# Performance work log

Measured on AMD Instinct MI355X. Metric: run time of the kernel, lower is better.

The kernel has to match this reference:

```python
import jax, jax.numpy as jnp
import numpy as np

EMBED = 1024
HEADS = 16
HEAD_DIM = EMBED // HEADS


def setup_inputs() -> dict:
    key = jax.random.key(0)
    ks = jax.random.split(key, 6)
    N, S = 4, 1024
    query = jax.random.normal(ks[0], (N, S, EMBED), dtype=jnp.float32)
    keys = jax.random.normal(ks[1], (N, S, EMBED), dtype=jnp.float32)
    values = jax.random.normal(ks[2], (N, S, EMBED), dtype=jnp.float32)
    mask = jax.random.randint(ks[3], (N, 1, S, S), 0, 2, dtype=jnp.int32)
    W_out = jax.random.normal(ks[4], (EMBED, EMBED), dtype=jnp.float32) * (1.0 / np.sqrt(EMBED))
    b_out = jax.random.normal(ks[5], (EMBED,), dtype=jnp.float32) * 0.02
    return {"query": query, "keys": keys, "values": values, "mask": mask,
            "W_out": W_out, "b_out": b_out}


def reference(query, keys, values, mask, W_out, b_out):
    N, Q, _ = query.shape
    K = keys.shape[1]
    # NOTE: the torch module never applies its per-head q/k/v Linear layers;
    # only the reshape + attention + fc_out are in the forward path.
    q = query.reshape(N, Q, HEADS, HEAD_DIM)
    k = keys.reshape(N, K, HEADS, HEAD_DIM)
    v = values.reshape(N, K, HEADS, HEAD_DIM)
    # energy: [N, H, Q, K]
    energy = jnp.einsum("bqhd,bkhd->bhqk", q, k)
    energy = jnp.where(mask == 0, jnp.float32(-1e20), energy)
    attn = jax.nn.softmax(energy / jnp.sqrt(jnp.float32(HEAD_DIM)), axis=3)
    out = jnp.einsum("bhqk,bkhd->bqhd", attn, v).reshape(N, Q, HEADS * HEAD_DIM)
    return out @ W_out.T + b_out
```

## Files before the change

kernel.cpp:

```cpp
#include <hip/hip_runtime.h>
#include <math.h>

#define NB 4
#define SL 1024
#define EMB 1024
#define NH 16
#define HD 64
#define QB 128

typedef __attribute__((ext_vector_type(8))) short bf16x8;
typedef __attribute__((ext_vector_type(4))) float f32x4;
typedef __attribute__((ext_vector_type(4))) unsigned u32x4;

static __device__ __forceinline__ unsigned pk2(float a, float b) {
    unsigned x = __float_as_uint(a) + 0x8000u;
    unsigned y = __float_as_uint(b) + 0x8000u;
    return (x >> 16) | (y & 0xFFFF0000u);
}
static __device__ __forceinline__ float exp2_fast(float x) {
    float r; asm("v_exp_f32 %0, %1" : "=v"(r) : "v"(x)); return r;
}
static __device__ __forceinline__ unsigned cvtpk(float a, float b) {
    unsigned r; asm("v_cvt_pk_bf16_f32 %0, %1, %2" : "=v"(r) : "v"(a), "v"(b)); return r;
}
static __device__ __forceinline__ void gload_lds16(const void* g, void* l) {
    __builtin_amdgcn_global_load_lds(
        (const __attribute__((address_space(1))) unsigned int*)g,
        (__attribute__((address_space(3))) unsigned int*)l, 16, 0, 0);
}

#define VMW(n) asm volatile("s_waitcnt vmcnt(" #n ")" ::: "memory")
#define MEMPIN() asm volatile("" ::: "memory")

__global__ __launch_bounds__(256) void prep(
    const float* __restrict__ W, unsigned short* __restrict__ Wb,
    const float* __restrict__ Kf, unsigned short* __restrict__ Kb,
    const float* __restrict__ V, unsigned short* __restrict__ Vt,
    const int* __restrict__ mask, unsigned long long* __restrict__ Mbt)
{
    __shared__ unsigned short sT[128 * 68];
    const int bid = blockIdx.x, tid = threadIdx.x;
    const float CSC = 0.125f * 1.44269504f;

    if (bid < 512) {
        int i = (bid * 256 + tid) * 8;
        float4 f0 = *(const float4*)&W[i];
        float4 f1 = *(const float4*)&W[i + 4];
        uint4 u = { pk2(f0.x,f0.y), pk2(f0.z,f0.w), pk2(f1.x,f1.y), pk2(f1.z,f1.w) };
        *(uint4*)&Wb[i] = u;
    } else if (bid < 2560) {
        int t = bid - 512;
        int b = t >> 9, h = (t >> 5) & 15, k0 = (t & 31) * 32;
        int r = tid >> 3, d = (tid & 7) * 8;
        const float* gp = &Kf[((size_t)(b * SL + k0 + r)) * EMB + h * HD + d];
        float4 f0 = *(const float4*)gp, f1 = *(const float4*)(gp + 4);
        uint4 u = { pk2(f0.x*CSC,f0.y*CSC), pk2(f0.z*CSC,f0.w*CSC),
                    pk2(f1.x*CSC,f1.y*CSC), pk2(f1.z*CSC,f1.w*CSC) };
        *(uint4*)&Kb[((size_t)((b * NH + h) * SL + k0 + r)) * HD + d] = u;
    } else if (bid < 3072) {
        int t = bid - 2560;
        int bh = t >> 3, kb = t & 7;
        int b = bh >> 4, h = bh & 15;
        int k0 = kb * 128;
        #pragma unroll
        for (int i = 0; i < 4; ++i) {
            int lin = (i * 256 + tid) * 8;
            int r = lin >> 6, d = lin & 63;
            const float* gp = &V[((size_t)(b * SL + k0 + r)) * EMB + h * HD + d];
            float4 f0 = *(const float4*)gp, f1 = *(const float4*)(gp + 4);
            uint2 u0 = { pk2(f0.x,f0.y), pk2(f0.z,f0.w) };
            uint2 u1 = { pk2(f1.x,f1.y), pk2(f1.z,f1.w) };
            *(uint2*)&sT[r * 68 + d]     = u0;
            *(uint2*)&sT[r * 68 + d + 4] = u1;
        }
        __syncthreads();
        #pragma unroll
        for (int p = 0; p < 4; ++p) {
            int d = p * 16 + (tid >> 4);
            int c = tid & 15;
            unsigned v[4];
            #pragma unroll
            for (int j = 0; j < 4; ++j) {
                unsigned lo = sT[(c * 8 + 2 * j) * 68 + d];
                unsigned hi = sT[(c * 8 + 2 * j + 1) * 68 + d];
                v[j] = lo | (hi << 16);
            }
            uint4 u = { v[0], v[1], v[2], v[3] };
            *(uint4*)&Vt[((size_t)(bh * HD + d)) * SL + k0 + c * 8] = u;
        }
    } else {
        int t = bid - 3072;
        int lane = tid & 63;
        #pragma unroll
        for (int r = 0; r < 4; ++r) {
            int wid = (t * 4 + (tid >> 6)) * 4 + r;
            int c = wid & 15, q = (wid >> 4) & 1023, bb = wid >> 14;
            int mv = mask[((size_t)bb * SL + q) * SL + c * 64 + lane];
            unsigned long long bits = __ballot(mv != 0);
            if (lane == 0) Mbt[((size_t)bb * 16 + c) * SL + q] = bits;
        }
    }
}

__global__ __launch_bounds__(512, 4) void attn_mfma(
    const float* __restrict__ Q, const unsigned short* __restrict__ Kb,
    const unsigned short* __restrict__ Vt,
    const unsigned long long* __restrict__ Mbt,
    unsigned short* __restrict__ Oa)
{
    const int lin = blockIdx.x;
    const int xcd = lin & 7, slot = lin >> 3;
    const int bh = xcd * 8 + (slot >> 3);
    const int q0 = (slot & 7) * QB;
    const int b = bh >> 4, h = bh & 15;
    const int tid = threadIdx.x;
    const int w = tid >> 6, lane = tid & 63;
    const int m16 = lane & 15, quad = lane >> 4;
    const int lr = lane >> 3, lc = lane & 7;
    const int grp = w >> 2;
    const int wq = w & 3;
    const int srow = w * 8;

    __shared__ __align__(16) unsigned short sAll[32768];
    unsigned short* sKb = sAll;
    unsigned short* sVb = sAll + 16384;

    const size_t vbase = (size_t)(bh * HD) * SL;
    const size_t kbase = (size_t)(bh * SL) * HD;
    const unsigned long long* Mp = Mbt + (size_t)(b * 16) * SL + q0 + wq * 32 + m16;

    float4 qf[2][4];
    #pragma unroll
    for (int u = 0; u < 2; ++u) {
        const float* qp = &Q[((size_t)(b * SL + q0 + wq * 32 + u * 16 + m16)) * EMB + h * HD + quad * 8];
        qf[u][0] = *(const float4*)qp;        qf[u][1] = *(const float4*)(qp + 4);
        qf[u][2] = *(const float4*)(qp + 32); qf[u][3] = *(const float4*)(qp + 36);
    }
    MEMPIN();
    #pragma unroll
    for (int t2 = 0; t2 < 2; ++t2) {
        gload_lds16(&Vt[vbase + (size_t)(srow + lr) * SL + t2 * 64 + (lc ^ lr) * 8],
                    &sVb[t2 * 4096 + srow * 64]);
        gload_lds16(&Kb[kbase + (size_t)(t2 * 64 + srow + lr) * HD + (lc ^ lr) * 8],
                    &sKb[t2 * 4096 + srow * 64]);
    }
    MEMPIN();
    unsigned long long mbC0 = Mp[(size_t)grp * SL];
    unsigned long long mbC1 = Mp[(size_t)grp * SL + 16];
    unsigned long long mbN0 = 0, mbN1 = 0;
    MEMPIN();

    bf16x8 bQ[2][2];
    #pragma unroll
    for (int u = 0; u < 2; ++u) {
        u32x4 u0 = { pk2(qf[u][0].x,qf[u][0].y), pk2(qf[u][0].z,qf[u][0].w),
                     pk2(qf[u][1].x,qf[u][1].y), pk2(qf[u][1].z,qf[u][1].w) };
        u32x4 u1 = { pk2(qf[u][2].x,qf[u][2].y), pk2(qf[u][2].z,qf[u][2].w),
                     pk2(qf[u][3].x,qf[u][3].y), pk2(qf[u][3].z,qf[u][3].w) };
        bQ[u][0] = __builtin_bit_cast(bf16x8, u0);
        bQ[u][1] = __builtin_bit_cast(bf16x8, u1);
    }

    f32x4 O[2][4] = {};
    f32x4 lacc[2] = {};
    const short one_bf = (short)0x3F80;
    const bf16x8 ones = { one_bf, one_bf, one_bf, one_bf, one_bf, one_bf, one_bf, one_bf };

    for (int i = 0; i < 8; ++i) {
        VMW(0);
        __builtin_amdgcn_s_barrier();
        __builtin_amdgcn_sched_barrier(0);

        const int t = 2 * i + grp;
        if (i < 7) {
            const int tE = 2 * i + 2;
            const int bE = tE & 3, bO = (tE + 1) & 3;
            gload_lds16(&Vt[vbase + (size_t)(srow + lr) * SL + tE * 64 + (lc ^ lr) * 8],
                        &sVb[bE * 4096 + srow * 64]);
            gload_lds16(&Kb[kbase + (size_t)(tE * 64 + srow + lr) * HD + (lc ^ lr) * 8],
                        &sKb[bE * 4096 + srow * 64]);
            gload_lds16(&Vt[vbase + (size_t)(srow + lr) * SL + (tE + 1) * 64 + (lc ^ lr) * 8],
                        &sVb[bO * 4096 + srow * 64]);
            gload_lds16(&Kb[kbase + (size_t)((tE + 1) * 64 + srow + lr) * HD + (lc ^ lr) * 8],
                        &sKb[bO * 4096 + srow * 64]);
            MEMPIN();
            mbN0 = Mp[(size_t)(t + 2) * SL];
            mbN1 = Mp[(size_t)(t + 2) * SL + 16];
            MEMPIN();
        }

        const unsigned short* kc = &sKb[(t & 3) * 4096];
        const unsigned short* vc = &sVb[(t & 3) * 4096];

        f32x4 sc[2][4];
        __builtin_amdgcn_s_setprio(1);
        #pragma unroll
        for (int t4 = 0; t4 < 4; ++t4) {
            int krow = t4 * 16 + m16;
            bf16x8 a0 = *(const bf16x8*)&kc[krow * 64 + ((quad ^ (krow & 7)) * 8)];
            bf16x8 a1 = *(const bf16x8*)&kc[krow * 64 + (((4 + quad) ^ (krow & 7)) * 8)];
            f32x4 z = {0.f, 0.f, 0.f, 0.f};
            sc[0][t4] = __builtin_amdgcn_mfma_f32_16x16x32_bf16(a0, bQ[0][0], z,         0,0,0);
            sc[0][t4] = __builtin_amdgcn_mfma_f32_16x16x32_bf16(a1, bQ[0][1], sc[0][t4], 0,0,0);
            sc[1][t4] = __builtin_amdgcn_mfma_f32_16x16x32_bf16(a0, bQ[1][0], z,         0,0,0);
            sc[1][t4] = __builtin_amdgcn_mfma_f32_16x16x32_bf16(a1, bQ[1][1], sc[1][t4], 0,0,0);
        }
        __builtin_amdgcn_s_setprio(0);

        bf16x8 bP[2][2];
        #pragma unroll
        for (int u = 0; u < 2; ++u) {
            unsigned long long mb = u ? mbC1 : mbC0;
            unsigned s0 = ((unsigned)mb) >> (quad * 8);
            unsigned s1 = ((unsigned)(mb >> 32)) >> (quad * 8);
            unsigned wt[4][2];
            #pragma unroll
            for (int t4 = 0; t4 < 4; ++t4) {
                wt[t4][0] = cvtpk(exp2_fast(sc[u][t4][0]), exp2_fast(sc[u][t4][1]));
                wt[t4][1] = cvtpk(exp2_fast(sc[u][t4][2]), exp2_fast(sc[u][t4][3]));
            }
            unsigned g[2][4];
            #pragma unroll
            for (int hh = 0; hh < 2; ++hh)
                #pragma unroll
                for (int p = 0; p < 2; ++p) {
                    unsigned A = wt[2 * hh][p], B = wt[2 * hh + 1][p];
                    asm("v_permlane32_swap_b32 %0, %1" : "+v"(A), "+v"(B));
                    asm("v_permlane16_swap_b32 %0, %1" : "+v"(A), "+v"(B));
                    g[hh][p] = A; g[hh][2 + p] = B;
                }
            #pragma unroll
            for (int hh = 0; hh < 2; ++hh) {
                unsigned sb = hh ? s1 : s0;
                #pragma unroll
                for (int j2 = 0; j2 < 4; ++j2) {
                    unsigned mlo = (unsigned)(((int)(sb << (31 - 2 * j2))) >> 31);
                    unsigned mhi = (unsigned)(((int)(sb << (30 - 2 * j2))) >> 31);
                    g[hh][j2] &= (mlo & 0xFFFFu) | (mhi & 0xFFFF0000u);
                }
            }
            u32x4 p0 = { g[0][0], g[0][1], g[0][2], g[0][3] };
            u32x4 p1 = { g[1][0], g[1][1], g[1][2], g[1][3] };
            bP[u][0] = __builtin_bit_cast(bf16x8, p0);
            bP[u][1] = __builtin_bit_cast(bf16x8, p1);
        }

        __builtin_amdgcn_s_setprio(1);
        lacc[0] = __builtin_amdgcn_mfma_f32_16x16x32_bf16(ones, bP[0][0], lacc[0], 0,0,0);
        lacc[0] = __builtin_amdgcn_mfma_f32_16x16x32_bf16(ones, bP[0][1], lacc[0], 0,0,0);
        lacc[1] = __builtin_amdgcn_mfma_f32_16x16x32_bf16(ones, bP[1][0], lacc[1], 0,0,0);
        lacc[1] = __builtin_amdgcn_mfma_f32_16x16x32_bf16(ones, bP[1][1], lacc[1], 0,0,0);

        #pragma unroll
        for (int dt = 0; dt < 4; ++dt) {
            int drow = dt * 16 + m16;
            bf16x8 v0 = *(const bf16x8*)&vc[drow * 64 + ((quad ^ (drow & 7)) * 8)];
            bf16x8 v1 = *(const bf16x8*)&vc[drow * 64 + (((4 + quad) ^ (drow & 7)) * 8)];
            O[0][dt] = __builtin_amdgcn_mfma_f32_16x16x32_bf16(v0, bP[0][0], O[0][dt], 0,0,0);
            O[0][dt] = __builtin_amdgcn_mfma_f32_16x16x32_bf16(v1, bP[0][1], O[0][dt], 0,0,0);
            O[1][dt] = __builtin_amdgcn_mfma_f32_16x16x32_bf16(v0, bP[1][0], O[1][dt], 0,0,0);
            O[1][dt] = __builtin_amdgcn_mfma_f32_16x16x32_bf16(v1, bP[1][1], O[1][dt], 0,0,0);
        }
        __builtin_amdgcn_s_setprio(0);

        mbC0 = mbN0; mbC1 = mbN1;
    }

    __syncthreads();
    float* sM = (float*)sAll;
    if (grp == 1) {
        #pragma unroll
        for (int u = 0; u < 2; ++u)
            #pragma unroll
            for (int dt = 0; dt < 4; ++dt)
                *(f32x4*)&sM[((u * 4 + dt) * 256 + wq * 64 + lane) * 4] = O[u][dt];
        sM[8192 + (wq * 64 + lane) * 2 + 0] = lacc[0][0];
        sM[8192 + (wq * 64 + lane) * 2 + 1] = lacc[1][0];
    }
    __syncthreads();
    if (grp == 0) {
        float l[2];
        l[0] = lacc[0][0] + sM[8192 + (wq * 64 + lane) * 2 + 0];
        l[1] = lacc[1][0] + sM[8192 + (wq * 64 + lane) * 2 + 1];
        #pragma unroll
        for (int u = 0; u < 2; ++u) {
            float inv = 1.f / l[u];
            size_t base = ((size_t)(b * SL + q0 + wq * 32 + u * 16 + m16)) * EMB + h * HD + quad * 4;
            #pragma unroll
            for (int dt = 0; dt < 4; ++dt) {
                f32x4 part = *(const f32x4*)&sM[((u * 4 + dt) * 256 + wq * 64 + lane) * 4];
                f32x4 o = O[u][dt] + part;
                uint2 ow = { cvtpk(o[0] * inv, o[1] * inv),
                             cvtpk(o[2] * inv, o[3] * inv) };
                *(uint2*)&Oa[base + dt * 16] = ow;
            }
        }
    }
}

__global__ __launch_bounds__(256, 3) void proj_mfma(
    const unsigned short* __restrict__ A, const unsigned short* __restrict__ Wb,
    const float* __restrict__ bias, float* __restrict__ C)
{
    const int lin = blockIdx.x;
    const int xcd = lin & 7, idx = lin >> 3;
    const int m0 = (xcd * 4 + (idx >> 4)) * 128;
    const int n0 = (idx & 15) * 64;
    const int tid = threadIdx.x;
    const int w = tid >> 6, lane = tid & 63;
    const int m16 = lane & 15, quad = lane >> 4;
    const int lr = lane >> 3, lc = lane & 7;
    const int wm = (w >> 1) * 64, wn = (w & 1) * 32;

    __shared__ __align__(16) unsigned short sA[2][128 * 64];
    __shared__ __align__(16) unsigned short sW[2][64 * 64];

    f32x4 acc[4][2] = {};

    #pragma unroll
    for (int i = 0; i < 4; ++i) {
        int r = w * 32 + i * 8;
        gload_lds16(&A[(size_t)(m0 + r + lr) * EMB + (lc ^ lr) * 8], &sA[0][r * 64]);
    }
    #pragma unroll
    for (int i = 0; i < 2; ++i) {
        int r = w * 16 + i * 8;
        gload_lds16(&Wb[(size_t)(n0 + r + lr) * EMB + (lc ^ lr) * 8], &sW[0][r * 64]);
    }
    __syncthreads();

    for (int it = 0; it < 16; ++it) {
        const int bf = it & 1;
        if (it < 15) {
            int e0 = (it + 1) * 64;
            #pragma unroll
            for (int i = 0; i < 4; ++i) {
                int r = w * 32 + i * 8;
                gload_lds16(&A[(size_t)(m0 + r + lr) * EMB + e0 + (lc ^ lr) * 8], &sA[bf ^ 1][r * 64]);
            }
            #pragma unroll
            for (int i = 0; i < 2; ++i) {
                int r = w * 16 + i * 8;
                gload_lds16(&Wb[(size_t)(n0 + r + lr) * EMB + e0 + (lc ^ lr) * 8], &sW[bf ^ 1][r * 64]);
            }
        }
        #pragma unroll
        for (int hh = 0; hh < 2; ++hh) {
            bf16x8 af[4], bw[2];
            #pragma unroll
            for (int mt = 0; mt < 4; ++mt) {
                int r = wm + mt * 16 + m16;
                af[mt] = *(const bf16x8*)&sA[bf][r * 64 + (((hh * 4 + quad) ^ (r & 7)) * 8)];
            }
            #pragma unroll
            for (int nt = 0; nt < 2; ++nt) {
                int r = wn + nt * 16 + m16;
                bw[nt] = *(const bf16x8*)&sW[bf][r * 64 + (((hh * 4 + quad) ^ (r & 7)) * 8)];
            }
            #pragma unroll
            for (int mt = 0; mt < 4; ++mt)
                #pragma unroll
                for (int nt = 0; nt < 2; ++nt)
                    acc[mt][nt] = __builtin_amdgcn_mfma_f32_16x16x32_bf16(af[mt], bw[nt], acc[mt][nt], 0,0,0);
        }
        __syncthreads();
    }

    #pragma unroll
    for (int nt = 0; nt < 2; ++nt) {
        float bv = bias[n0 + wn + nt * 16 + m16];
        #pragma unroll
        for (int mt = 0; mt < 4; ++mt) {
            size_t row = (size_t)(m0 + wm + mt * 16 + quad * 4);
            #pragma unroll
            for (int rg = 0; rg < 4; ++rg)
                C[(row + rg) * EMB + n0 + wn + nt * 16 + m16] = acc[mt][nt][rg] + bv;
        }
    }
}

extern "C" void kernel_launch(void* const* d_in, const int* in_sizes, int n_in,
                              void* d_out, int out_size, void* d_ws, size_t ws_size,
                              hipStream_t stream) {
    const float* Q    = (const float*)d_in[0];
    const float* K    = (const float*)d_in[1];
    const float* V    = (const float*)d_in[2];
    const int*   mask = (const int*)  d_in[3];
    const float* W    = (const float*)d_in[4];
    const float* bias = (const float*)d_in[5];

    unsigned short* Oa = (unsigned short*)d_ws;
    unsigned short* Wb = Oa + (size_t)NB * SL * EMB;
    unsigned long long* Mbt = (unsigned long long*)(Wb + (size_t)EMB * EMB);
    unsigned short* Vt = (unsigned short*)(Mbt + (size_t)NB * 16 * SL);
    unsigned short* Kb = Vt + (size_t)NB * NH * HD * SL;

    prep<<<7168, 256, 0, stream>>>(W, Wb, K, Kb, V, Vt, mask, Mbt);
    attn_mfma<<<512, 512, 0, stream>>>(Q, Kb, Vt, Mbt, Oa);
    proj_mfma<<<512, 256, 0, stream>>>(Oa, Wb, bias, (float*)d_out);
}
```

Measured before the change: 155.2 us.

## Triple-buffer projection GEMM loads and relax attention loop vmcnt wait

The output projection kernel moves from a double-buffered to a three-stage LDS pipeline. It issues loads two tiles ahead and replaces the trailing __syncthreads with a partial vmcnt wait plus barrier at the top of each iteration. Launch bounds drop to 2 blocks per CU because of the larger LDS footprint. The attention kernel's loop-top wait is relaxed from vmcnt(0) to vmcnt(2), so the mask prefetch loads can remain outstanding. This hides more global load latency, at the cost of occupancy and some risk of reading LDS before its data has arrived.

```diff
diff --git a/kernel.cpp b/kernel.cpp
--- a/kernel.cpp
+++ b/kernel.cpp
@@ -167,7 +167,7 @@
     const bf16x8 ones = { one_bf, one_bf, one_bf, one_bf, one_bf, one_bf, one_bf, one_bf };
 
     for (int i = 0; i < 8; ++i) {
-        VMW(0);
+        VMW(2);
         __builtin_amdgcn_s_barrier();
         __builtin_amdgcn_sched_barrier(0);
 
@@ -298,7 +298,7 @@
     }
 }
 
-__global__ __launch_bounds__(256, 3) void proj_mfma(
+__global__ __launch_bounds__(256, 2) void proj_mfma(
     const unsigned short* __restrict__ A, const unsigned short* __restrict__ Wb,
     const float* __restrict__ bias, float* __restrict__ C)
 {
@@ -312,38 +312,45 @@
     const int lr = lane >> 3, lc = lane & 7;
     const int wm = (w >> 1) * 64, wn = (w & 1) * 32;
 
-    __shared__ __align__(16) unsigned short sA[2][128 * 64];
-    __shared__ __align__(16) unsigned short sW[2][64 * 64];
+    __shared__ __align__(16) unsigned short sA[3][128 * 64];
+    __shared__ __align__(16) unsigned short sW[3][64 * 64];
 
     f32x4 acc[4][2] = {};
 
-    #pragma unroll
-    for (int i = 0; i < 4; ++i) {
-        int r = w * 32 + i * 8;
-        gload_lds16(&A[(size_t)(m0 + r + lr) * EMB + (lc ^ lr) * 8], &sA[0][r * 64]);
-    }
-    #pragma unroll
-    for (int i = 0; i < 2; ++i) {
-        int r = w * 16 + i * 8;
-        gload_lds16(&Wb[(size_t)(n0 + r + lr) * EMB + (lc ^ lr) * 8], &sW[0][r * 64]);
-    }
-    __syncthreads();
+    #define PSTAGE(IT, BI)                                                        \
+    {                                                                             \
+        const int e0_ = (IT) * 64;                                                \
+        _Pragma("unroll")                                                         \
+        for (int i_ = 0; i_ < 4; ++i_) {                                          \
+            int r_ = w * 32 + i_ * 8;                                             \
+            gload_lds16(&A[(size_t)(m0 + r_ + lr) * EMB + e0_ + (lc ^ lr) * 8],   \
+                        &sA[BI][r_ * 64]);                                        \
+        }                                                                         \
+        _Pragma("unroll")                                                         \
+        for (int i_ = 0; i_ < 2; ++i_) {                                          \
+            int r_ = w * 16 + i_ * 8;                                             \
+            gload_lds16(&Wb[(size_t)(n0 + r_ + lr) * EMB + e0_ + (lc ^ lr) * 8],  \
+                        &sW[BI][r_ * 64]);                                        \
+        }                                                                         \
+    }
+
+    PSTAGE(0, 0)
+    MEMPIN();
+    PSTAGE(1, 1)
+    MEMPIN();
 
     for (int it = 0; it < 16; ++it) {
-        const int bf = it & 1;
-        if (it < 15) {
-            int e0 = (it + 1) * 64;
-            #pragma unroll
-            for (int i = 0; i < 4; ++i) {
-                int r = w * 32 + i * 8;
-                gload_lds16(&A[(size_t)(m0 + r + lr) * EMB + e0 + (lc ^ lr) * 8], &sA[bf ^ 1][r * 64]);
-            }
-            #pragma unroll
-            for (int i = 0; i < 2; ++i) {
-                int r = w * 16 + i * 8;
-                gload_lds16(&Wb[(size_t)(n0 + r + lr) * EMB + e0 + (lc ^ lr) * 8], &sW[bf ^ 1][r * 64]);
-            }
-        }
+        if (it < 15) { VMW(6); } else { VMW(0); }
+        __builtin_amdgcn_s_barrier();
+        __builtin_amdgcn_sched_barrier(0);
+
+        if (it < 14) {
+            const int bn = (it + 2) % 3;
+            PSTAGE(it + 2, bn)
+            MEMPIN();
+        }
+
+        const int bf = it % 3;
         #pragma unroll
         for (int hh = 0; hh < 2; ++hh) {
             bf16x8 af[4], bw[2];
@@ -363,7 +370,6 @@
                 for (int nt = 0; nt < 2; ++nt)
                     acc[mt][nt] = __builtin_amdgcn_mfma_f32_16x16x32_bf16(af[mt], bw[nt], acc[mt][nt], 0,0,0);
         }
-        __syncthreads();
     }
 
     #pragma unroll
```

Result: faster. 151.1 us (median of 2 runs) (-2.6%).
